# Optimization experiments

Measured on AMD Instinct MI355X. Metric: run time of the kernel, lower is better.

Reference implementation:

```python
import jax, jax.numpy as jnp
import numpy as np

N, M, FEAT, POS, D, MSG, NCLS = 64, 32, 256, 6, 262, 128, 7


def setup_inputs() -> dict:
    key = jax.random.key(0)
    ks = jax.random.split(key, 12)
    s = 0.05
    p = lambda k, shape: jax.random.normal(k, shape, jnp.float32) * s
    return {
        "nodes_feature": jax.random.normal(ks[0], (N, M, FEAT), jnp.float32),
        "pos": jax.random.normal(ks[1], (N, M, POS), jnp.float32),
        "num_rec": jax.random.randint(ks[2], (N,), 1, M + 1),
        "link_w1": p(ks[3], (D, 2 * D)),
        "link_b1": jnp.zeros((D,), jnp.float32),
        "link_w2": p(ks[4], (D,)),
        "link_b2": jnp.zeros((), jnp.float32),
        "msg_w": p(ks[5], (MSG, D)),
        "msg_b": jnp.zeros((MSG,), jnp.float32),
        "gru_w_ih": p(ks[6], (3 * D, MSG)),
        "gru_w_hh": p(ks[7], (3 * D, D)),
        "gru_b_ih": jnp.zeros((3 * D,), jnp.float32),
        "gru_b_hh": jnp.zeros((3 * D,), jnp.float32),
        "ro_w1": p(ks[8], (MSG, D)),
        "ro_b1": jnp.zeros((MSG,), jnp.float32),
        "ro_w2": p(ks[9], (NCLS, MSG)),
        "ro_b2": jnp.zeros((NCLS,), jnp.float32),
    }


def reference(nodes_feature, pos, num_rec, link_w1, link_b1, link_w2, link_b2,
              msg_w, msg_b, gru_w_ih, gru_w_hh, gru_b_ih, gru_b_hh,
              ro_w1, ro_b1, ro_w2, ro_b2):
    # node_feat = [resnet_feat, pos]  -> (N, M, 262)
    nf = jnp.concatenate([nodes_feature, pos], axis=-1)
    n, m, d = nf.shape
    valid = jnp.arange(m)[None, :] < num_rec[:, None]          # (N, M)
    pair = valid[:, :, None] & valid[:, None, :]               # (N, M, M)

    # edge_feat[b,:,i,j] = concat(nf[b,i], nf[b,j]); zero for invalid pairs
    ef = jnp.concatenate([
        jnp.broadcast_to(nf[:, :, None, :], (n, m, m, d)),
        jnp.broadcast_to(nf[:, None, :, :], (n, m, m, d)),
    ], axis=-1) * pair[..., None].astype(nf.dtype)             # (N, M, M, 2D)

    # 1x1 convs == per-pair MLP
    hlink = jax.nn.relu(jnp.einsum('bnwc,dc->bnwd', ef, link_w1) + link_b1)
    attmat = jax.nn.sigmoid(jnp.einsum('bnwd,d->bnw', hlink, link_w2) + link_b2)

    # messages are only summed over valid sender nodes w
    att_m = attmat * valid[:, None, :].astype(attmat.dtype)    # (N, M, M)

    def gru_step(x, h):
        # PyTorch GRU cell: gates order (r, z, n)
        gx = x @ gru_w_ih.T + gru_b_ih
        gh = h @ gru_w_hh.T + gru_b_hh
        xr, xz, xn = jnp.split(gx, 3, axis=-1)
        hr, hz, hn = jnp.split(gh, 3, axis=-1)
        r = jax.nn.sigmoid(xr + hr)
        z = jax.nn.sigmoid(xz + hz)
        c = jnp.tanh(xn + r * hn)
        return (1.0 - z) * c + z * h

    vmask = valid[..., None].astype(nf.dtype)
    h_state = nf                                               # pass 0 input state
    for _ in range(2):                                         # two message-passing rounds
        msg = h_state @ msg_w.T + msg_b                        # (N, M, 128)
        m_v = jnp.einsum('bnw,bwk->bnk', att_m, msg)           # attention-weighted sum
        h_state = gru_step(m_v, h_state) * vmask               # invalid nodes stay zero

    pred = (jax.nn.relu(h_state @ ro_w1.T + ro_b1) @ ro_w2.T + ro_b2) * vmask
    return pred, attmat
```

## Files before the change

### kernel.cpp

```cpp
#include <hip/hip_runtime.h>
#include <math.h>

#define N_G   64
#define M_N   32
#define FEAT  256
#define POSD  6
#define D     262
#define MSG   128
#define NCLS  7

#define KA_S  424
#define KHW   288
#define KFULL 416
#define PSTR  320

#define S_PROJ (528*288)
#define S_MSG  (128*288)
#define S_RZ   (544*416)
#define S_XN   (272*128)
#define S_HN   (272*288)
#define S_RO   (128*288)
#define S_RO2  (16*128)

#define O_WPROJ 0u
#define O_WMSG  76032u
#define O_WRZ   94464u
#define O_WXN   207616u
#define O_WHN   225024u
#define O_WRO   264192u
#define O_WRO2  282624u
#define O_GB    283648u

typedef __attribute__((ext_vector_type(8))) short short8;
typedef __attribute__((ext_vector_type(4))) short short4v;
typedef __attribute__((ext_vector_type(4))) float floatx4;

#define MFMA __builtin_amdgcn_mfma_f32_16x16x32_bf16

__device__ __forceinline__ short f2bf(float f) {
    union { float f; unsigned u; } v; v.f = f;
    unsigned r = v.u + 0x7FFF + ((v.u >> 16) & 1);
    return (short)(r >> 16);
}
__device__ __forceinline__ float bf2f(short s) {
    union { float f; unsigned u; } v;
    v.u = ((unsigned)(unsigned short)s) << 16;
    return v.f;
}
__device__ __forceinline__ float sigf(float x) { return 1.f / (1.f + expf(-x)); }

__global__ void prep_kernel(const float* __restrict__ w1, const float* __restrict__ msg_w,
                            const float* __restrict__ w_ih, const float* __restrict__ w_hh,
                            const float* __restrict__ ro_w1, const float* __restrict__ ro_w2,
                            const float* __restrict__ b_ih, const float* __restrict__ b_hh,
                            float* __restrict__ ws)
{
    short* wproj = (short*)(ws + O_WPROJ);
    short* wmsg  = (short*)(ws + O_WMSG);
    short* wrz   = (short*)(ws + O_WRZ);
    short* wxn   = (short*)(ws + O_WXN);
    short* whn   = (short*)(ws + O_WHN);
    short* wro   = (short*)(ws + O_WRO);
    short* wro2  = (short*)(ws + O_WRO2);
    float* gb    = ws + O_GB;
    const int TOT_S = S_PROJ + S_MSG + S_RZ + S_XN + S_HN + S_RO + S_RO2;
    const int TOTAL = TOT_S + 1088;
    for (int i = blockIdx.x * blockDim.x + threadIdx.x; i < TOTAL;
         i += gridDim.x * blockDim.x) {
        int idx = i;
        if (idx < S_PROJ) {
            int n = idx / 288, k = idx % 288;
            float v = 0.f;
            if (k < D && n < 524)
                v = (n < D) ? w1[n * 524 + k] : w1[(n - D) * 524 + D + k];
            wproj[idx] = f2bf(v);
            continue;
        }
        idx -= S_PROJ;
        if (idx < S_MSG) {
            int n = idx / 288, k = idx % 288;
            wmsg[idx] = f2bf(k < D ? msg_w[n * D + k] : 0.f);
            continue;
        }
        idx -= S_MSG;
        if (idx < S_RZ) {
            int g = idx / 416, k = idx % 416;
            int gi = (g < 272) ? 0 : 1;
            int d = g - gi * 272;
            float v = 0.f;
            if (d < D) {
                int row = gi * D + d;
                if (k < 128)            v = w_ih[row * MSG + k];
                else if (k < 128 + D)   v = w_hh[row * D + (k - 128)];
            }
            wrz[idx] = f2bf(v);
            continue;
        }
        idx -= S_RZ;
        if (idx < S_XN) {
            int d = idx / 128, k = idx % 128;
            wxn[idx] = f2bf(d < D ? w_ih[(2 * D + d) * MSG + k] : 0.f);
            continue;
        }
        idx -= S_XN;
        if (idx < S_HN) {
            int d = idx / 288, k = idx % 288;
            whn[idx] = f2bf((d < D && k < D) ? w_hh[(2 * D + d) * D + k] : 0.f);
            continue;
        }
        idx -= S_HN;
        if (idx < S_RO) {
            int n = idx / 288, k = idx % 288;
            wro[idx] = f2bf(k < D ? ro_w1[n * D + k] : 0.f);
            continue;
        }
        idx -= S_RO;
        if (idx < S_RO2) {
            int n = idx / 128, k = idx % 128;
            wro2[idx] = f2bf(n < NCLS ? ro_w2[n * MSG + k] : 0.f);
            continue;
        }
        idx -= S_RO2;
        {
            int seg = idx / 272, d = idx % 272;
            float v = 0.f;
            if (d < D) {
                if (seg == 0)      v = b_ih[d] + b_hh[d];
                else if (seg == 1) v = b_ih[D + d] + b_hh[D + d];
                else if (seg == 2) v = b_ih[2 * D + d];
                else               v = b_hh[2 * D + d];
            }
            gb[idx] = v;
        }
    }
}

__global__ __launch_bounds__(512, 2) void fused_kernel(
    const float* __restrict__ nodes, const float* __restrict__ pos,
    const int* __restrict__ nrec_g,
    const float* __restrict__ b1g, const float* __restrict__ w2g,
    const float* __restrict__ b2g, const float* __restrict__ msg_bg,
    const float* __restrict__ ro_b1g, const float* __restrict__ ro_b2g,
    const float* __restrict__ ws,
    float* __restrict__ att_out, float* __restrict__ pred)
{
    const short* Wproj = (const short*)(ws + O_WPROJ);
    const short* Wmsg  = (const short*)(ws + O_WMSG);
    const short* Wrz   = (const short*)(ws + O_WRZ);
    const short* Wxn   = (const short*)(ws + O_WXN);
    const short* Whn   = (const short*)(ws + O_WHN);
    const short* Wro   = (const short*)(ws + O_WRO);
    const short* Wro2  = (const short*)(ws + O_WRO2);
    const float* gb    = ws + O_GB;

    __shared__ __align__(16) short bufA[32 * KA_S];
    __shared__ __align__(16) short bufB[32 * KA_S];
    __shared__ __align__(16) short paL[32 * PSTR];
    __shared__ __align__(16) short pbL[32 * PSTR];
    __shared__ __align__(16) short attL[32 * 40];
    __shared__ __align__(16) short msgT[128 * 40];
    __shared__ __align__(16) short hidL[32 * 136];
    __shared__ __align__(16) float b1L[PSTR], w2L[PSTR];

    const int b = blockIdx.x;
    const int tid = threadIdx.x;
    const int wave = tid >> 6, lane = tid & 63;
    const int quad = lane >> 4, lrow = lane & 15;
    const int nr = nrec_g[b];

    for (int idx = tid; idx < 32 * 64; idx += 512) {
        int w = idx >> 6, c4 = idx & 63;
        floatx4 v = *(const floatx4*)(nodes + ((size_t)(b * 32 + w)) * FEAT + c4 * 4);
        short4v s; s[0] = f2bf(v[0]); s[1] = f2bf(v[1]); s[2] = f2bf(v[2]); s[3] = f2bf(v[3]);
        *(short4v*)(bufA + w * KA_S + 128 + c4 * 4) = s;
    }
    for (int idx = tid; idx < 32 * POSD; idx += 512) {
        int w = idx / POSD, c = idx % POSD;
        bufA[w * KA_S + 128 + FEAT + c] = f2bf(pos[((size_t)(b * 32 + w)) * POSD + c]);
    }
    for (int idx = tid; idx < 32 * 34; idx += 512) {
        int w = idx / 34, c = idx % 34;
        bufA[w * KA_S + 390 + c] = 0;
        bufB[w * KA_S + 390 + c] = 0;
    }
    for (int idx = tid; idx < 32 * (PSTR - D); idx += 512) {
        int w = idx / (PSTR - D), c = idx % (PSTR - D);
        paL[w * PSTR + D + c] = 0;
        pbL[w * PSTR + D + c] = 0;
    }
    for (int d = tid; d < PSTR; d += 512) {
        b1L[d] = (d < D) ? b1g[d] : 0.f;
        w2L[d] = (d < D) ? w2g[d] : 0.f;
    }
    __syncthreads();

    for (int s = wave; s < 33; s += 8) {
        floatx4 acc0 = {}, acc1 = {};
        const short* bw = Wproj + (s * 16 + lrow) * KHW + quad * 8;
        const short* ap = bufA + lrow * KA_S + 128 + quad * 8;
        for (int kk = 0; kk < 9; ++kk) {
            short8 a0 = *(const short8*)(ap + kk * 32);
            short8 a1 = *(const short8*)(ap + 16 * KA_S + kk * 32);
            short8 bv = *(const short8*)(bw + kk * 32);
            acc0 = MFMA(a0, bv, acc0, 0, 0, 0);
            acc1 = MFMA(a1, bv, acc1, 0, 0, 0);
        }
        int col = s * 16 + lrow;
#pragma unroll
        for (int rr = 0; rr < 4; ++rr) {
            int r0 = quad * 4 + rr;
            if (col < D) {
                paL[r0 * PSTR + col] = f2bf(acc0[rr]);
                paL[(r0 + 16) * PSTR + col] = f2bf(acc1[rr]);
            } else if (col < 2 * D) {
                pbL[r0 * PSTR + (col - D)] = f2bf(acc0[rr]);
                pbL[(r0 + 16) * PSTR + (col - D)] = f2bf(acc1[rr]);
            }
        }
    }
    __syncthreads();

    {
        const int grp = tid >> 4;
        const int c16 = tid & 15;
        const float b2v = b2g[0];
        float pav[5][4], b1v[5][4], w2v[5][4];
#pragma unroll
        for (int k = 0; k < 5; ++k) {
            int dbase = c16 * 4 + 64 * k;
            short4v p = *(const short4v*)(paL + grp * PSTR + dbase);
            floatx4 bb = *(const floatx4*)(b1L + dbase);
            floatx4 ww = *(const floatx4*)(w2L + dbase);
#pragma unroll
            for (int e = 0; e < 4; ++e) {
                pav[k][e] = bf2f(p[e]); b1v[k][e] = bb[e]; w2v[k][e] = ww[e];
            }
        }
        float p0 = 0.f;
#pragma unroll
        for (int k = 0; k < 5; ++k)
#pragma unroll
            for (int e = 0; e < 4; ++e)
                p0 += fmaxf(b1v[k][e], 0.f) * w2v[k][e];
        p0 += __shfl_down(p0, 8, 16); p0 += __shfl_down(p0, 4, 16);
        p0 += __shfl_down(p0, 2, 16); p0 += __shfl_down(p0, 1, 16);
        float c0 = sigf(p0 + b2v);
        const bool vi = grp < nr;
        for (int j = 0; j < 32; ++j) {
            float a;
            if (j < nr && vi) {
                const short* pb = pbL + j * PSTR + c16 * 4;
                float s = 0.f;
#pragma unroll
                for (int k = 0; k < 5; ++k) {
                    short4v q = *(const short4v*)(pb + 64 * k);
#pragma unroll
                    for (int e = 0; e < 4; ++e) {
                        float v = pav[k][e] + bf2f(q[e]) + b1v[k][e];
                        s += fmaxf(v, 0.f) * w2v[k][e];
                    }
                }
                s += __shfl_down(s, 8, 16); s += __shfl_down(s, 4, 16);
                s += __shfl_down(s, 2, 16); s += __shfl_down(s, 1, 16);
                a = sigf(s + b2v);
            } else {
                a = c0;
            }
            if (c16 == 0) {
                att_out[((size_t)(b * 32 + grp)) * 32 + j] = a;
                attL[grp * 40 + j] = f2bf((j < nr) ? a : 0.f);
            }
        }
    }
    __syncthreads();

    for (int rnd = 0; rnd < 2; ++rnd) {
        short* src = rnd ? bufB : bufA;
        short* dst = rnd ? bufA : bufB;

        {
            int s = wave;
            floatx4 acc0 = {}, acc1 = {};
            const short* bw = Wmsg + (s * 16 + lrow) * KHW + quad * 8;
            const short* ap = src + lrow * KA_S + 128 + quad * 8;
            for (int kk = 0; kk < 9; ++kk) {
                short8 a0 = *(const short8*)(ap + kk * 32);
                short8 a1 = *(const short8*)(ap + 16 * KA_S + kk * 32);
                short8 bv = *(const short8*)(bw + kk * 32);
                acc0 = MFMA(a0, bv, acc0, 0, 0, 0);
                acc1 = MFMA(a1, bv, acc1, 0, 0, 0);
            }
            int col = s * 16 + lrow;
            float bias = msg_bg[col];
#pragma unroll
            for (int rr = 0; rr < 4; ++rr) {
                msgT[col * 40 + quad * 4 + rr] = f2bf(acc0[rr] + bias);
                msgT[col * 40 + 16 + quad * 4 + rr] = f2bf(acc1[rr] + bias);
            }
        }
        __syncthreads();

        {
            int mi = wave & 1, ng = wave >> 1;
            short8 afrag = *(const short8*)(attL + (mi * 16 + lrow) * 40 + quad * 8);
            floatx4 acc0 = {}, acc1 = {};
            short8 bf0 = *(const short8*)(msgT + (ng * 32 + lrow) * 40 + quad * 8);
            short8 bf1 = *(const short8*)(msgT + (ng * 32 + 16 + lrow) * 40 + quad * 8);
            acc0 = MFMA(afrag, bf0, acc0, 0, 0, 0);
            acc1 = MFMA(afrag, bf1, acc1, 0, 0, 0);
#pragma unroll
            for (int rr = 0; rr < 4; ++rr) {
                int m = mi * 16 + quad * 4 + rr;
                src[m * KA_S + ng * 32 + lrow] = f2bf(acc0[rr]);
                src[m * KA_S + ng * 32 + 16 + lrow] = f2bf(acc1[rr]);
            }
        }
        __syncthreads();

        for (int s = wave; s < 17; s += 8) {
            floatx4 aR0 = {}, aR1 = {}, aZ0 = {}, aZ1 = {};
            floatx4 aN0 = {}, aN1 = {}, aH0 = {}, aH1 = {};
            const short* ap  = src + lrow * KA_S + quad * 8;
            const short* bpr = Wrz + (s * 16 + lrow) * KFULL + quad * 8;
            const short* bpz = Wrz + (272 + s * 16 + lrow) * KFULL + quad * 8;
            const short* bpx = Wxn + (s * 16 + lrow) * 128 + quad * 8;
            const short* bph = Whn + (s * 16 + lrow) * KHW + quad * 8;
            for (int kk = 0; kk < 13; ++kk) {
                short8 a0 = *(const short8*)(ap + kk * 32);
                short8 a1 = *(const short8*)(ap + 16 * KA_S + kk * 32);
                short8 br = *(const short8*)(bpr + kk * 32);
                short8 bz = *(const short8*)(bpz + kk * 32);
                aR0 = MFMA(a0, br, aR0, 0, 0, 0);
                aR1 = MFMA(a1, br, aR1, 0, 0, 0);
                aZ0 = MFMA(a0, bz, aZ0, 0, 0, 0);
                aZ1 = MFMA(a1, bz, aZ1, 0, 0, 0);
                if (kk < 4) {
                    short8 bx = *(const short8*)(bpx + kk * 32);
                    aN0 = MFMA(a0, bx, aN0, 0, 0, 0);
                    aN1 = MFMA(a1, bx, aN1, 0, 0, 0);
                } else {
                    short8 bh = *(const short8*)(bph + (kk - 4) * 32);
                    aH0 = MFMA(a0, bh, aH0, 0, 0, 0);
                    aH1 = MFMA(a1, bh, aH1, 0, 0, 0);
                }
            }
            int d = s * 16 + lrow;
            if (d < D) {
                float bgr = gb[d], bgz = gb[272 + d];
                float bxv = gb[544 + d], bhv = gb[816 + d];
#pragma unroll
                for (int i = 0; i < 2; ++i) {
                    floatx4 vR = i ? aR1 : aR0, vZ = i ? aZ1 : aZ0;
                    floatx4 vN = i ? aN1 : aN0, vH = i ? aH1 : aH0;
#pragma unroll
                    for (int rr = 0; rr < 4; ++rr) {
                        int m = i * 16 + quad * 4 + rr;
                        float rg = sigf(vR[rr] + bgr);
                        float zg = sigf(vZ[rr] + bgz);
                        float cg = tanhf(vN[rr] + bxv + rg * (vH[rr] + bhv));
                        float hold = bf2f(src[m * KA_S + 128 + d]);
                        float hv = (1.f - zg) * cg + zg * hold;
                        if (m >= nr) hv = 0.f;
                        dst[m * KA_S + 128 + d] = f2bf(hv);
                    }
                }
            }
        }
        __syncthreads();
    }

    {
        int s = wave;
        floatx4 acc0 = {}, acc1 = {};
        const short* bw = Wro + (s * 16 + lrow) * KHW + quad * 8;
        const short* ap = bufA + lrow * KA_S + 128 + quad * 8;
        for (int kk = 0; kk < 9; ++kk) {
            short8 a0 = *(const short8*)(ap + kk * 32);
            short8 a1 = *(const short8*)(ap + 16 * KA_S + kk * 32);
            short8 bv = *(const short8*)(bw + kk * 32);
            acc0 = MFMA(a0, bv, acc0, 0, 0, 0);
            acc1 = MFMA(a1, bv, acc1, 0, 0, 0);
        }
        int col = s * 16 + lrow;
        float bias = ro_b1g[col];
#pragma unroll
        for (int rr = 0; rr < 4; ++rr) {
            hidL[(quad * 4 + rr) * 136 + col] = f2bf(fmaxf(acc0[rr] + bias, 0.f));
            hidL[(16 + quad * 4 + rr) * 136 + col] = f2bf(fmaxf(acc1[rr] + bias, 0.f));
        }
    }
    __syncthreads();

    if (wave == 0) {
        floatx4 acc0 = {}, acc1 = {};
        const short* ap = hidL + lrow * 136 + quad * 8;
        const short* bw = Wro2 + lrow * 128 + quad * 8;
        for (int kk = 0; kk < 4; ++kk) {
            short8 a0 = *(const short8*)(ap + kk * 32);
            short8 a1 = *(const short8*)(ap + 16 * 136 + kk * 32);
            short8 bv = *(const short8*)(bw + kk * 32);
            acc0 = MFMA(a0, bv, acc0, 0, 0, 0);
            acc1 = MFMA(a1, bv, acc1, 0, 0, 0);
        }
        int q = lrow;
        if (q < NCLS) {
            float bias = ro_b2g[q];
#pragma unroll
            for (int i = 0; i < 2; ++i) {
#pragma unroll
                for (int rr = 0; rr < 4; ++rr) {
                    int m = i * 16 + quad * 4 + rr;
                    float v = (i ? acc1[rr] : acc0[rr]) + bias;
                    if (m >= nr) v = 0.f;
                    pred[((size_t)(b * 32 + m)) * NCLS + q] = v;
                }
            }
        }
    }
}

extern "C" void kernel_launch(void* const* d_in, const int* in_sizes, int n_in,
                              void* d_out, int out_size, void* d_ws, size_t ws_size,
                              hipStream_t stream)
{
    const float* nodes = (const float*)d_in[0];
    const float* pos   = (const float*)d_in[1];
    const int*   nrec  = (const int*)d_in[2];
    const float* w1    = (const float*)d_in[3];
    const float* b1    = (const float*)d_in[4];
    const float* w2    = (const float*)d_in[5];
    const float* b2    = (const float*)d_in[6];
    const float* msg_w = (const float*)d_in[7];
    const float* msg_b = (const float*)d_in[8];
    const float* w_ih  = (const float*)d_in[9];
    const float* w_hh  = (const float*)d_in[10];
    const float* b_ih  = (const float*)d_in[11];
    const float* b_hh  = (const float*)d_in[12];
    const float* ro_w1 = (const float*)d_in[13];
    const float* ro_b1 = (const float*)d_in[14];
    const float* ro_w2 = (const float*)d_in[15];
    const float* ro_b2 = (const float*)d_in[16];
    float* ws   = (float*)d_ws;
    float* pred = (float*)d_out;
    float* attout = pred + (size_t)N_G * M_N * NCLS;

    prep_kernel<<<256, 256, 0, stream>>>(w1, msg_w, w_ih, w_hh, ro_w1, ro_w2,
                                         b_ih, b_hh, ws);
    fused_kernel<<<N_G, 512, 0, stream>>>(nodes, pos, nrec, b1, w2, b2, msg_b,
                                          ro_b1, ro_b2, ws, attout, pred);
}
```

Before: 160.4 us.

## Double block to 1024 threads, fuse round-0 message GEMM into projection, fast sigmoid/tanh

Raises the per-graph block from 512 to 1024 threads and splits each GEMM's 32 rows into two 16-row halves so twice as many waves share the projection, GRU, and readout work. The round-0 message projection is folded into the first projection loop, which removes one GEMM phase and one barrier. Sigmoid and tanh now use __expf plus the hardware reciprocal instead of expf, tanhf and division. The aim is more parallelism per graph, since only 64 blocks run. The cost is a higher register cap pressure per thread and less reuse of B fragments across rows.

```diff
diff --git a/kernel.cpp b/kernel.cpp
--- a/kernel.cpp
+++ b/kernel.cpp
@@ -47,7 +47,14 @@
     v.u = ((unsigned)(unsigned short)s) << 16;
     return v.f;
 }
-__device__ __forceinline__ float sigf(float x) { return 1.f / (1.f + expf(-x)); }
+__device__ __forceinline__ float sigf(float x) {
+    return __builtin_amdgcn_rcpf(1.f + __expf(-x));
+}
+__device__ __forceinline__ float tanh_fast(float x) {
+    float e = __expf(-2.f * fabsf(x));
+    float t = (1.f - e) * __builtin_amdgcn_rcpf(1.f + e);
+    return copysignf(t, x);
+}
 
 __global__ void prep_kernel(const float* __restrict__ w1, const float* __restrict__ msg_w,
                             const float* __restrict__ w_ih, const float* __restrict__ w_hh,
@@ -135,7 +142,7 @@
     }
 }
 
-__global__ __launch_bounds__(512, 2) void fused_kernel(
+__global__ __launch_bounds__(1024) void fused_kernel(
     const float* __restrict__ nodes, const float* __restrict__ pos,
     const int* __restrict__ nrec_g,
     const float* __restrict__ b1g, const float* __restrict__ w2g,
@@ -168,35 +175,37 @@
     const int quad = lane >> 4, lrow = lane & 15;
     const int nr = nrec_g[b];
 
-    for (int idx = tid; idx < 32 * 64; idx += 512) {
+    for (int idx = tid; idx < 32 * 64; idx += 1024) {
         int w = idx >> 6, c4 = idx & 63;
         floatx4 v = *(const floatx4*)(nodes + ((size_t)(b * 32 + w)) * FEAT + c4 * 4);
         short4v s; s[0] = f2bf(v[0]); s[1] = f2bf(v[1]); s[2] = f2bf(v[2]); s[3] = f2bf(v[3]);
         *(short4v*)(bufA + w * KA_S + 128 + c4 * 4) = s;
     }
-    for (int idx = tid; idx < 32 * POSD; idx += 512) {
+    for (int idx = tid; idx < 32 * POSD; idx += 1024) {
         int w = idx / POSD, c = idx % POSD;
         bufA[w * KA_S + 128 + FEAT + c] = f2bf(pos[((size_t)(b * 32 + w)) * POSD + c]);
     }
-    for (int idx = tid; idx < 32 * 34; idx += 512) {
+    for (int idx = tid; idx < 32 * 34; idx += 1024) {
         int w = idx / 34, c = idx % 34;
         bufA[w * KA_S + 390 + c] = 0;
         bufB[w * KA_S + 390 + c] = 0;
     }
-    for (int idx = tid; idx < 32 * (PSTR - D); idx += 512) {
+    for (int idx = tid; idx < 32 * (PSTR - D); idx += 1024) {
         int w = idx / (PSTR - D), c = idx % (PSTR - D);
         paL[w * PSTR + D + c] = 0;
         pbL[w * PSTR + D + c] = 0;
     }
-    for (int d = tid; d < PSTR; d += 512) {
+    for (int d = tid; d < PSTR; d += 1024) {
         b1L[d] = (d < D) ? b1g[d] : 0.f;
         w2L[d] = (d < D) ? w2g[d] : 0.f;
     }
     __syncthreads();
 
-    for (int s = wave; s < 33; s += 8) {
+    for (int s = wave; s < 41; s += 16) {
         floatx4 acc0 = {}, acc1 = {};
-        const short* bw = Wproj + (s * 16 + lrow) * KHW + quad * 8;
+        const short* bw = (s < 33)
+            ? Wproj + (s * 16 + lrow) * KHW + quad * 8
+            : Wmsg + ((s - 33) * 16 + lrow) * KHW + quad * 8;
         const short* ap = bufA + lrow * KA_S + 128 + quad * 8;
         for (int kk = 0; kk < 9; ++kk) {
             short8 a0 = *(const short8*)(ap + kk * 32);
@@ -205,16 +214,26 @@
             acc0 = MFMA(a0, bv, acc0, 0, 0, 0);
             acc1 = MFMA(a1, bv, acc1, 0, 0, 0);
         }
-        int col = s * 16 + lrow;
-#pragma unroll
-        for (int rr = 0; rr < 4; ++rr) {
-            int r0 = quad * 4 + rr;
-            if (col < D) {
-                paL[r0 * PSTR + col] = f2bf(acc0[rr]);
-                paL[(r0 + 16) * PSTR + col] = f2bf(acc1[rr]);
-            } else if (col < 2 * D) {
-                pbL[r0 * PSTR + (col - D)] = f2bf(acc0[rr]);
-                pbL[(r0 + 16) * PSTR + (col - D)] = f2bf(acc1[rr]);
+        if (s < 33) {
+            int col = s * 16 + lrow;
+#pragma unroll
+            for (int rr = 0; rr < 4; ++rr) {
+                int r0 = quad * 4 + rr;
+                if (col < D) {
+                    paL[r0 * PSTR + col] = f2bf(acc0[rr]);
+                    paL[(r0 + 16) * PSTR + col] = f2bf(acc1[rr]);
+                } else if (col < 2 * D) {
+                    pbL[r0 * PSTR + (col - D)] = f2bf(acc0[rr]);
+                    pbL[(r0 + 16) * PSTR + (col - D)] = f2bf(acc1[rr]);
+                }
+            }
+        } else {
+            int col = (s - 33) * 16 + lrow;
+            float bias = msg_bg[col];
+#pragma unroll
+            for (int rr = 0; rr < 4; ++rr) {
+                msgT[col * 40 + quad * 4 + rr] = f2bf(acc0[rr] + bias);
+                msgT[col * 40 + 16 + quad * 4 + rr] = f2bf(acc1[rr] + bias);
             }
         }
     }
@@ -222,13 +241,15 @@
 
     {
         const int grp = tid >> 4;
+        const int i   = grp >> 1;
+        const int jh  = (grp & 1) * 16;
         const int c16 = tid & 15;
         const float b2v = b2g[0];
         float pav[5][4], b1v[5][4], w2v[5][4];
 #pragma unroll
         for (int k = 0; k < 5; ++k) {
             int dbase = c16 * 4 + 64 * k;
-            short4v p = *(const short4v*)(paL + grp * PSTR + dbase);
+            short4v p = *(const short4v*)(paL + i * PSTR + dbase);
             floatx4 bb = *(const floatx4*)(b1L + dbase);
             floatx4 ww = *(const floatx4*)(w2L + dbase);
 #pragma unroll
@@ -245,8 +266,9 @@
         p0 += __shfl_down(p0, 8, 16); p0 += __shfl_down(p0, 4, 16);
         p0 += __shfl_down(p0, 2, 16); p0 += __shfl_down(p0, 1, 16);
         float c0 = sigf(p0 + b2v);
-        const bool vi = grp < nr;
-        for (int j = 0; j < 32; ++j) {
+        const bool vi = i < nr;
+        for (int jj = 0; jj < 16; ++jj) {
+            int j = jh + jj;
             float a;
             if (j < nr && vi) {
                 const short* pb = pbL + j * PSTR + c16 * 4;
@@ -267,8 +289,8 @@
                 a = c0;
             }
             if (c16 == 0) {
-                att_out[((size_t)(b * 32 + grp)) * 32 + j] = a;
-                attL[grp * 40 + j] = f2bf((j < nr) ? a : 0.f);
+                att_out[((size_t)(b * 32 + i)) * 32 + j] = a;
+                attL[i * 40 + j] = f2bf((j < nr) ? a : 0.f);
             }
         }
     }
@@ -278,70 +300,58 @@
         short* src = rnd ? bufB : bufA;
         short* dst = rnd ? bufA : bufB;
 
-        {
-            int s = wave;
-            floatx4 acc0 = {}, acc1 = {};
+        if (rnd) {
+            int s = wave >> 1, mi = wave & 1;
+            floatx4 acc = {};
             const short* bw = Wmsg + (s * 16 + lrow) * KHW + quad * 8;
-            const short* ap = src + lrow * KA_S + 128 + quad * 8;
+            const short* ap = src + (mi * 16 + lrow) * KA_S + 128 + quad * 8;
             for (int kk = 0; kk < 9; ++kk) {
                 short8 a0 = *(const short8*)(ap + kk * 32);
-                short8 a1 = *(const short8*)(ap + 16 * KA_S + kk * 32);
                 short8 bv = *(const short8*)(bw + kk * 32);
-                acc0 = MFMA(a0, bv, acc0, 0, 0, 0);
-                acc1 = MFMA(a1, bv, acc1, 0, 0, 0);
+                acc = MFMA(a0, bv, acc, 0, 0, 0);
             }
             int col = s * 16 + lrow;
             float bias = msg_bg[col];
 #pragma unroll
-            for (int rr = 0; rr < 4; ++rr) {
-                msgT[col * 40 + quad * 4 + rr] = f2bf(acc0[rr] + bias);
-                msgT[col * 40 + 16 + quad * 4 + rr] = f2bf(acc1[rr] + bias);
-            }
-        }
-        __syncthreads();
+            for (int rr = 0; rr < 4; ++rr)
+                msgT[col * 40 + mi * 16 + quad * 4 + rr] = f2bf(acc[rr] + bias);
+            __syncthreads();
+        }
 
         {
             int mi = wave & 1, ng = wave >> 1;
             short8 afrag = *(const short8*)(attL + (mi * 16 + lrow) * 40 + quad * 8);
-            floatx4 acc0 = {}, acc1 = {};
-            short8 bf0 = *(const short8*)(msgT + (ng * 32 + lrow) * 40 + quad * 8);
-            short8 bf1 = *(const short8*)(msgT + (ng * 32 + 16 + lrow) * 40 + quad * 8);
-            acc0 = MFMA(afrag, bf0, acc0, 0, 0, 0);
-            acc1 = MFMA(afrag, bf1, acc1, 0, 0, 0);
+            floatx4 acc = {};
+            short8 bf0 = *(const short8*)(msgT + (ng * 16 + lrow) * 40 + quad * 8);
+            acc = MFMA(afrag, bf0, acc, 0, 0, 0);
 #pragma unroll
             for (int rr = 0; rr < 4; ++rr) {
                 int m = mi * 16 + quad * 4 + rr;
-                src[m * KA_S + ng * 32 + lrow] = f2bf(acc0[rr]);
-                src[m * KA_S + ng * 32 + 16 + lrow] = f2bf(acc1[rr]);
+                src[m * KA_S + ng * 16 + lrow] = f2bf(acc[rr]);
             }
         }
         __syncthreads();
 
-        for (int s = wave; s < 17; s += 8) {
-            floatx4 aR0 = {}, aR1 = {}, aZ0 = {}, aZ1 = {};
-            floatx4 aN0 = {}, aN1 = {}, aH0 = {}, aH1 = {};
-            const short* ap  = src + lrow * KA_S + quad * 8;
+        for (int u = wave; u < 34; u += 16) {
+            int s = u >> 1, half = u & 1;
+            floatx4 aR = {}, aZ = {}, aN = {}, aH = {};
+            const short* ap  = src + (half * 16 + lrow) * KA_S + quad * 8;
             const short* bpr = Wrz + (s * 16 + lrow) * KFULL + quad * 8;
             const short* bpz = Wrz + (272 + s * 16 + lrow) * KFULL + quad * 8;
             const short* bpx = Wxn + (s * 16 + lrow) * 128 + quad * 8;
             const short* bph = Whn + (s * 16 + lrow) * KHW + quad * 8;
             for (int kk = 0; kk < 13; ++kk) {
                 short8 a0 = *(const short8*)(ap + kk * 32);
-                short8 a1 = *(const short8*)(ap + 16 * KA_S + kk * 32);
                 short8 br = *(const short8*)(bpr + kk * 32);
                 short8 bz = *(const short8*)(bpz + kk * 32);
-                aR0 = MFMA(a0, br, aR0, 0, 0, 0);
-                aR1 = MFMA(a1, br, aR1, 0, 0, 0);
-                aZ0 = MFMA(a0, bz, aZ0, 0, 0, 0);
-                aZ1 = MFMA(a1, bz, aZ1, 0, 0, 0);
+                aR = MFMA(a0, br, aR, 0, 0, 0);
+                aZ = MFMA(a0, bz, aZ, 0, 0, 0);
                 if (kk < 4) {
                     short8 bx = *(const short8*)(bpx + kk * 32);
-                    aN0 = MFMA(a0, bx, aN0, 0, 0, 0);
-                    aN1 = MFMA(a1, bx, aN1, 0, 0, 0);
+                    aN = MFMA(a0, bx, aN, 0, 0, 0);
                 } else {
                     short8 bh = *(const short8*)(bph + (kk - 4) * 32);
-                    aH0 = MFMA(a0, bh, aH0, 0, 0, 0);
-                    aH1 = MFMA(a1, bh, aH1, 0, 0, 0);
+                    aH = MFMA(a0, bh, aH, 0, 0, 0);
                 }
             }
             int d = s * 16 + lrow;
@@ -349,20 +359,15 @@
                 float bgr = gb[d], bgz = gb[272 + d];
                 float bxv = gb[544 + d], bhv = gb[816 + d];
 #pragma unroll
-                for (int i = 0; i < 2; ++i) {
-                    floatx4 vR = i ? aR1 : aR0, vZ = i ? aZ1 : aZ0;
-                    floatx4 vN = i ? aN1 : aN0, vH = i ? aH1 : aH0;
-#pragma unroll
-                    for (int rr = 0; rr < 4; ++rr) {
-                        int m = i * 16 + quad * 4 + rr;
-                        float rg = sigf(vR[rr] + bgr);
-                        float zg = sigf(vZ[rr] + bgz);
-                        float cg = tanhf(vN[rr] + bxv + rg * (vH[rr] + bhv));
-                        float hold = bf2f(src[m * KA_S + 128 + d]);
-                        float hv = (1.f - zg) * cg + zg * hold;
-                        if (m >= nr) hv = 0.f;
-                        dst[m * KA_S + 128 + d] = f2bf(hv);
-                    }
+                for (int rr = 0; rr < 4; ++rr) {
+                    int m = half * 16 + quad * 4 + rr;
+                    float rg = sigf(aR[rr] + bgr);
+                    float zg = sigf(aZ[rr] + bgz);
+                    float cg = tanh_fast(aN[rr] + bxv + rg * (aH[rr] + bhv));
+                    float hold = bf2f(src[m * KA_S + 128 + d]);
+                    float hv = (1.f - zg) * cg + zg * hold;
+                    if (m >= nr) hv = 0.f;
+                    dst[m * KA_S + 128 + d] = f2bf(hv);
                 }
             }
         }
@@ -370,50 +375,41 @@
     }
 
     {
-        int s = wave;
-        floatx4 acc0 = {}, acc1 = {};
+        int s = wave >> 1, mi = wave & 1;
+        floatx4 acc = {};
         const short* bw = Wro + (s * 16 + lrow) * KHW + quad * 8;
-        const short* ap = bufA + lrow * KA_S + 128 + quad * 8;
+        const short* ap = bufA + (mi * 16 + lrow) * KA_S + 128 + quad * 8;
         for (int kk = 0; kk < 9; ++kk) {
             short8 a0 = *(const short8*)(ap + kk * 32);
-            short8 a1 = *(const short8*)(ap + 16 * KA_S + kk * 32);
             short8 bv = *(const short8*)(bw + kk * 32);
-            acc0 = MFMA(a0, bv, acc0, 0, 0, 0);
-            acc1 = MFMA(a1, bv, acc1, 0, 0, 0);
+            acc = MFMA(a0, bv, acc, 0, 0, 0);
         }
         int col = s * 16 + lrow;
         float bias = ro_b1g[col];
 #pragma unroll
-        for (int rr = 0; rr < 4; ++rr) {
-            hidL[(quad * 4 + rr) * 136 + col] = f2bf(fmaxf(acc0[rr] + bias, 0.f));
-            hidL[(16 + quad * 4 + rr) * 136 + col] = f2bf(fmaxf(acc1[rr] + bias, 0.f));
-        }
+        for (int rr = 0; rr < 4; ++rr)
+            hidL[(mi * 16 + quad * 4 + rr) * 136 + col] = f2bf(fmaxf(acc[rr] + bias, 0.f));
     }
     __syncthreads();
 
-    if (wave == 0) {
-        floatx4 acc0 = {}, acc1 = {};
-        const short* ap = hidL + lrow * 136 + quad * 8;
+    if (wave < 2) {
+        floatx4 acc = {};
+        const short* ap = hidL + (wave * 16 + lrow) * 136 + quad * 8;
         const short* bw = Wro2 + lrow * 128 + quad * 8;
         for (int kk = 0; kk < 4; ++kk) {
             short8 a0 = *(const short8*)(ap + kk * 32);
-            short8 a1 = *(const short8*)(ap + 16 * 136 + kk * 32);
             short8 bv = *(const short8*)(bw + kk * 32);
-            acc0 = MFMA(a0, bv, acc0, 0, 0, 0);
-            acc1 = MFMA(a1, bv, acc1, 0, 0, 0);
+            acc = MFMA(a0, bv, acc, 0, 0, 0);
         }
         int q = lrow;
         if (q < NCLS) {
             float bias = ro_b2g[q];
 #pragma unroll
-            for (int i = 0; i < 2; ++i) {
-#pragma unroll
-                for (int rr = 0; rr < 4; ++rr) {
-                    int m = i * 16 + quad * 4 + rr;
-                    float v = (i ? acc1[rr] : acc0[rr]) + bias;
-                    if (m >= nr) v = 0.f;
-                    pred[((size_t)(b * 32 + m)) * NCLS + q] = v;
-                }
+            for (int rr = 0; rr < 4; ++rr) {
+                int m = wave * 16 + quad * 4 + rr;
+                float v = acc[rr] + bias;
+                if (m >= nr) v = 0.f;
+                pred[((size_t)(b * 32 + m)) * NCLS + q] = v;
             }
         }
     }
@@ -446,6 +442,6 @@
 
     prep_kernel<<<256, 256, 0, stream>>>(w1, msg_w, w_ih, w_hh, ro_w1, ro_w2,
                                          b_ih, b_hh, ws);
-    fused_kernel<<<N_G, 512, 0, stream>>>(nodes, pos, nrec, b1, w2, b2, msg_b,
-                                          ro_b1, ro_b2, ws, attout, pred);
-}
+    fused_kernel<<<N_G, 1024, 0, stream>>>(nodes, pos, nrec, b1, w2, b2, msg_b,
+                                           ro_b1, ro_b2, ws, attout, pred);
+}
```

Result: no change. 162.1 us (+1.0%).
